# Optimization experiments

Hardware: AMD Instinct MI355X
Metric: run time of the kernel (lower is better)

The kernel has to match this reference:

```python
import jax, jax.numpy as jnp
import numpy as np

T, B, I, H = 512, 128, 256, 256
P = 0.25          # fixed dropout rate (float branch of p_logit)
EPS = 1e-07
TEMP = 0.1


def _concrete_mask(u, p):
    # (1 - sigmoid((log(p+eps)-log(1-p+eps)+log(u+eps)-log(1-u+eps))/t)) / (1-p)
    logit_p = jnp.log(p + EPS) - jnp.log(1.0 - p + EPS)
    logit_u = jnp.log(u + EPS) - jnp.log(1.0 - u + EPS)
    return (1.0 - jax.nn.sigmoid((logit_p + logit_u) / TEMP)) / (1.0 - p)


def setup_inputs() -> dict:
    key = jax.random.key(0)
    ks = jax.random.split(key, 7)
    k_scale = 1.0 / np.sqrt(H)  # matches uniform(-k, k) scale in init_weights
    inp = {
        "input": jax.random.normal(ks[0], (T, B, I), dtype=jnp.float32),
        "ux": jax.random.uniform(ks[1], (4, B, I), dtype=jnp.float32),
        "uh": jax.random.uniform(ks[2], (4, B, H), dtype=jnp.float32),
        "W": jax.random.normal(ks[3], (4, H, I), dtype=jnp.float32) * k_scale,
        "Wb": jax.random.normal(ks[4], (4, H), dtype=jnp.float32) * k_scale,
        "U": jax.random.normal(ks[5], (4, H, H), dtype=jnp.float32) * k_scale,
        "Ub": jax.random.normal(ks[6], (4, H), dtype=jnp.float32) * k_scale,
    }
    return inp


def reference(input, ux, uh, W, Wb, U, Ub):
    # Dropout masks (sampled once, shared across all timesteps), gate order i,f,o,g
    zx = _concrete_mask(ux, P)  # (4, B, I)
    zh = _concrete_mask(uh, P)  # (4, B, H)

    # Input-side gate pre-activations for ALL timesteps at once:
    # x_g[t] = (input[t] * zx[g]) @ W[g].T + Wb[g]  -> (T, B, 4, H)
    xm = input[:, None, :, :] * zx[None]                 # (T, 4, B, I)
    x_pre = jnp.einsum("tgbi,ghi->tbgh", xm, W) + Wb     # (T, B, 4, H)

    h0 = jnp.zeros((B, H), dtype=input.dtype)
    c0 = jnp.zeros((B, H), dtype=input.dtype)

    def step(carry, pre_t):
        h, c = carry
        hm = h[None] * zh                                 # (4, B, H)
        s = pre_t + jnp.einsum("gbh,gkh->bgk", hm, U) + Ub  # (B, 4, H)
        i = jax.nn.sigmoid(s[:, 0])
        f = jax.nn.sigmoid(s[:, 1])
        o = jax.nn.sigmoid(s[:, 2])
        g = jnp.tanh(s[:, 3])
        c = f * c + i * g
        h = o * jnp.tanh(c)
        return (h, c), h

    (h_t, c_t), hn = jax.lax.scan(step, (h0, c0), x_pre)
    return hn, h_t, c_t
```

## Files before the change

### kernel.cpp

```cpp
#include <hip/hip_runtime.h>
#include <hip/hip_bf16.h>

#define T_STEPS 512
#define B_SZ    128
#define I_SZ    256
#define H_SZ    256
#define NB      16
#define SCAN_BLOCKS (B_SZ / NB)
#define SCAN_THREADS 512

typedef __attribute__((ext_vector_type(8))) short short8;
typedef __attribute__((ext_vector_type(4))) float floatx4;
union I4S8 { uint4 u; short8 s; };

#define HM_G_STRIDE 8320
#define ST_OFF      33280
#define ST_ROW      268
#define ULDS_OFF    (ST_OFF + 64 * ST_ROW * 4)
#define ULDS_W      7168
#define SMEM_BYTES  (ULDS_OFF + 8 * ULDS_W)

static constexpr int SORD[8][8] = {
    {-1,-1,-1,-1,-1, 0, 2, 4},
    {-1,-1,-1,-1,-1, 1, 3, 5},
    {-1,-1,-1,-1,-1, 6, 8,10},
    {-1,-1,-1,-1,-1, 7, 9,11},
    {-1,-1,-1,-1,-1,12,14,16},
    {-1,-1,-1,-1,-1,13,15,17},
    {-1,-1,-1,-1,-1,19,21,23},
    {-1,-1,-1,-1,18,20,22,24},
};
static constexpr int SFRG[25] = {
     5,13, 6,14, 7,15,
    21,29,22,30,23,31,
    37,45,38,46,39,47,
    60,53,61,54,62,55,63
};

__device__ __forceinline__ float fast_sigmoid(float x) {
    return 1.f / (1.f + __expf(-x));
}
__device__ __forceinline__ float fast_tanh(float x) {
    float ax = fabsf(x);
    float e = __expf(-2.f * ax);
    float t = (1.f - e) / (1.f + e);
    return copysignf(t, x);
}
__device__ __forceinline__ ushort f2bf(float v) {
    __hip_bfloat16 hb = __float2bfloat16(v);
    return *(ushort*)&hb;
}
__device__ __forceinline__ float bf2f(ushort u) {
    unsigned int b = ((unsigned int)u) << 16;
    return __uint_as_float(b);
}
__device__ __forceinline__ float concrete_mask(float u) {
    const float EPS = 1e-7f;
    float logit_p = logf(0.25f + EPS) - logf(0.75f + EPS);
    float lu = logf(u + EPS) - logf(1.0f - u + EPS);
    float z = (logit_p + lu) * 10.0f;
    float sig = 1.0f / (1.0f + expf(-z));
    return (1.0f - sig) * (1.0f / 0.75f);
}

__device__ __forceinline__ void barrier_lds_only() {
    asm volatile("s_waitcnt lgkmcnt(0)" ::: "memory");
    __builtin_amdgcn_s_barrier();
    asm volatile("" ::: "memory");
}

__global__ void mask_kernel(const float* __restrict__ ux, const float* __restrict__ uh,
                            float* __restrict__ zx, __hip_bfloat16* __restrict__ zh) {
    int idx = blockIdx.x * blockDim.x + threadIdx.x;
    const int n = 4 * B_SZ * I_SZ;
    if (idx < n) zx[idx] = concrete_mask(ux[idx]);
    else         zh[idx - n] = __float2bfloat16(concrete_mask(uh[idx - n]));
}

__global__ void uswz_kernel(const float* __restrict__ M, __hip_bfloat16* __restrict__ M_sw) {
    int tId = blockIdx.x * 256 + threadIdx.x;
    int lane  = tId & 63;
    int kk    = (tId >> 6) & 7;
    int ktile = (tId >> 9) & 15;
    int g     = tId >> 13;
    int nCol  = ktile * 16 + (lane & 15);
    int h0    = kk * 32 + ((lane >> 4) & 3) * 8;
    const float* src = M + ((size_t)g * 256 + nCol) * 256 + h0;
    ushort o[8];
    #pragma unroll
    for (int j = 0; j < 8; ++j) o[j] = f2bf(src[j]);
    uint4 pk;
    pk.x = (uint)o[0] | ((uint)o[1] << 16);
    pk.y = (uint)o[2] | ((uint)o[3] << 16);
    pk.z = (uint)o[4] | ((uint)o[5] << 16);
    pk.w = (uint)o[6] | ((uint)o[7] << 16);
    ((uint4*)M_sw)[tId] = pk;
}

__global__ __launch_bounds__(512, 2) void xpre_mfma_kernel(
        const float* __restrict__ input, const float* __restrict__ zx,
        const __hip_bfloat16* __restrict__ W_sw,
        const float* __restrict__ Wb, const float* __restrict__ Ub,
        __hip_bfloat16* __restrict__ xpre) {
    const int tid   = threadIdx.x;
    const int w     = tid >> 6;
    const int lane  = tid & 63;
    const int g     = w >> 1;
    const int khalf = w & 1;
    const int row0  = blockIdx.x * 64;
    const int mrow  = lane & 15;
    const int kq    = lane >> 4;

    floatx4 acc[4][8];
    #pragma unroll
    for (int mt = 0; mt < 4; ++mt)
        #pragma unroll
        for (int nt = 0; nt < 8; ++nt)
            #pragma unroll
            for (int r = 0; r < 4; ++r) acc[mt][nt][r] = 0.f;

    const uint4* Wp = (const uint4*)W_sw + ((size_t)((g * 16 + khalf * 8) * 8)) * 64 + lane;

    for (int kc = 0; kc < 8; ++kc) {
        I4S8 af[4];
        const int i0 = kc * 32 + kq * 8;
        #pragma unroll
        for (int mt = 0; mt < 4; ++mt) {
            int row = row0 + mt * 16 + mrow;
            int b   = row & (B_SZ - 1);
            const float4* ip = (const float4*)(input + (size_t)row * I_SZ + i0);
            const float4* zp = (const float4*)(zx + ((size_t)g * B_SZ + b) * I_SZ + i0);
            float4 a0 = ip[0], a1 = ip[1];
            float4 z0 = zp[0], z1 = zp[1];
            uint4 pk;
            pk.x = (uint)f2bf(a0.x * z0.x) | ((uint)f2bf(a0.y * z0.y) << 16);
            pk.y = (uint)f2bf(a0.z * z0.z) | ((uint)f2bf(a0.w * z0.w) << 16);
            pk.z = (uint)f2bf(a1.x * z1.x) | ((uint)f2bf(a1.y * z1.y) << 16);
            pk.w = (uint)f2bf(a1.z * z1.z) | ((uint)f2bf(a1.w * z1.w) << 16);
            af[mt].u = pk;
        }
        #pragma unroll
        for (int nt = 0; nt < 8; ++nt) {
            I4S8 bb; bb.u = Wp[(nt * 8 + kc) * 64];
            #pragma unroll
            for (int mt = 0; mt < 4; ++mt)
                acc[mt][nt] = __builtin_amdgcn_mfma_f32_16x16x32_bf16(af[mt].s, bb.s, acc[mt][nt], 0, 0, 0);
        }
    }
    #pragma unroll
    for (int nt = 0; nt < 8; ++nt) {
        int col = khalf * 128 + nt * 16 + (lane & 15);
        float bias = Wb[g * H_SZ + col] + Ub[g * H_SZ + col];
        #pragma unroll
        for (int mt = 0; mt < 4; ++mt) {
            #pragma unroll
            for (int r = 0; r < 4; ++r) {
                int row = row0 + mt * 16 + (lane >> 4) * 4 + r;
                xpre[((size_t)row * 4 + g) * H_SZ + col] = __float2bfloat16(acc[mt][nt][r] + bias);
            }
        }
    }
}

__global__ __launch_bounds__(SCAN_THREADS, 2) void scan_mfma_kernel(
        const __hip_bfloat16* __restrict__ xpre,
        const __hip_bfloat16* __restrict__ zh,
        const __hip_bfloat16* __restrict__ U_sw,
        float* __restrict__ out) {
    extern __shared__ __align__(16) char smem[];
    const int tid  = threadIdx.x;
    const int b0   = blockIdx.x * NB;
    const int w     = tid >> 6;
    const int lane  = tid & 63;
    const int g_w   = w >> 1;
    const int khalf = w & 1;
    const int be      = tid >> 5;
    const int k8      = (tid & 31) * 8;
    const int kk_e    = k8 >> 5;
    const int lane_hm = (be & 15) | (((k8 >> 3) & 3) << 4);
    const int sw_e    = ((be >> 2) & 1) << 4;

    const uint4* Uw = (const uint4*)U_sw + ((size_t)((g_w * 16 + khalf * 8) * 8)) * 64 + lane;
    float* st = (float*)(smem + ST_OFF);

    uint4 ures[32];
    #pragma unroll
    for (int nt = 0; nt < 8; ++nt)
        #pragma unroll
        for (int kk = 0; kk < 4; ++kk)
            ures[nt * 4 + kk] = Uw[(nt * 8 + kk) * 64];
    #pragma unroll
    for (int f = 0; f < 7; ++f) {
        uint4 v = Uw[(f * 8 + 4) * 64];
        *(uint4*)(smem + ULDS_OFF + w * ULDS_W + f * 1024 + lane * 16) = v;
    }
    for (int i = tid; i < HM_G_STRIDE * 4 / 16; i += SCAN_THREADS)
        ((uint4*)smem)[i] = make_uint4(0u, 0u, 0u, 0u);

    uint4 zhreg[4];
    float c8[8], h8[8];
    #pragma unroll
    for (int g = 0; g < 4; ++g)
        zhreg[g] = *(const uint4*)(zh + ((size_t)g * B_SZ + (b0 + be)) * H_SZ + k8);
    #pragma unroll
    for (int j = 0; j < 8; ++j) c8[j] = 0.f;

    uint4 xpn[4];
    #pragma unroll
    for (int g = 0; g < 4; ++g)
        xpn[g] = *(const uint4*)(xpre + (((size_t)0 * B_SZ + (b0 + be)) * 4 + g) * H_SZ + k8);
    uint4 sbuf[4];
    #pragma unroll
    for (int q = 0; q < 4; ++q) sbuf[q] = Uw[SFRG[q] * 64];

    __syncthreads();

    for (int t = 0; t < T_STEPS; ++t) {
        I4S8 afr[8];
        #pragma unroll
        for (int kk = 0; kk < 8; ++kk)
            afr[kk].u = *(const uint4*)(smem + g_w * HM_G_STRIDE + kk * 1040 + lane * 16);

        #pragma unroll
        for (int p = 0; p < 4; ++p) {
            floatx4 acc[2];
            #pragma unroll
            for (int e = 0; e < 2; ++e)
                #pragma unroll
                for (int r = 0; r < 4; ++r) acc[e][r] = 0.f;

            uint4 lb[2];
            #pragma unroll
            for (int e = 0; e < 2; ++e) {
                const int nt = 2 * p + e;
                if (nt < 7)
                    lb[e] = *(const uint4*)(smem + ULDS_OFF + w * ULDS_W + nt * 1024 + lane * 16);
            }

            #pragma unroll
            for (int kk = 0; kk < 8; ++kk) {
                #pragma unroll
                for (int e = 0; e < 2; ++e) {
                    const int nt = 2 * p + e;
                    I4S8 bb;
                    if (kk < 4) {
                        bb.u = ures[nt * 4 + kk];
                    } else if (kk == 4 && nt < 7) {
                        bb.u = lb[e];
                    } else {
                        const int o = SORD[nt][kk];
                        bb.u = sbuf[o & 3];
                        if (o + 4 < 25) sbuf[o & 3] = Uw[SFRG[o + 4] * 64];
                    }
                    acc[e] = __builtin_amdgcn_mfma_f32_16x16x32_bf16(afr[kk].s, bb.s, acc[e], 0, 0, 0);
                }
            }
            #pragma unroll
            for (int e = 0; e < 2; ++e) {
                const int nt = 2 * p + e;
                int kcol  = khalf * 128 + nt * 16 + (lane & 15);
                int kswz  = kcol ^ (((lane >> 4) & 1) << 4);
                int brow4 = (lane >> 4) * 4;
                #pragma unroll
                for (int r = 0; r < 4; ++r)
                    st[((brow4 + r) * 4 + g_w) * ST_ROW + kswz] = acc[e][r];
            }
        }
        barrier_lds_only();

        float sg[4][8];
        #pragma unroll
        for (int g = 0; g < 4; ++g) {
            const float* strow = st + ((be * 4 + g) * ST_ROW + (k8 ^ sw_e));
            float4 lo = *(const float4*)(strow);
            float4 hi = *(const float4*)(strow + 4);
            sg[g][0] = lo.x; sg[g][1] = lo.y; sg[g][2] = lo.z; sg[g][3] = lo.w;
            sg[g][4] = hi.x; sg[g][5] = hi.y; sg[g][6] = hi.z; sg[g][7] = hi.w;
            const ushort* xs = (const ushort*)&xpn[g];
            #pragma unroll
            for (int j = 0; j < 8; ++j) sg[g][j] += bf2f(xs[j]);
        }
        {
            const int tn = (t + 1 < T_STEPS) ? t + 1 : t;
            #pragma unroll
            for (int g = 0; g < 4; ++g)
                xpn[g] = *(const uint4*)(xpre + (((size_t)tn * B_SZ + (b0 + be)) * 4 + g) * H_SZ + k8);
        }
        #pragma unroll
        for (int j = 0; j < 8; ++j) {
            float iv = fast_sigmoid(sg[0][j]);
            float fv = fast_sigmoid(sg[1][j]);
            float ov = fast_sigmoid(sg[2][j]);
            float gv = fast_tanh(sg[3][j]);
            float c  = fv * c8[j] + iv * gv;
            c8[j] = c;
            h8[j] = ov * fast_tanh(c);
        }
        {
            float* op = out + ((size_t)t * B_SZ + (b0 + be)) * H_SZ + k8;
            *(float4*)(op)     = make_float4(h8[0], h8[1], h8[2], h8[3]);
            *(float4*)(op + 4) = make_float4(h8[4], h8[5], h8[6], h8[7]);
        }
        #pragma unroll
        for (int g = 0; g < 4; ++g) {
            const ushort* zs = (const ushort*)&zhreg[g];
            uint4 pk;
            pk.x = (uint)f2bf(h8[0] * bf2f(zs[0])) | ((uint)f2bf(h8[1] * bf2f(zs[1])) << 16);
            pk.y = (uint)f2bf(h8[2] * bf2f(zs[2])) | ((uint)f2bf(h8[3] * bf2f(zs[3])) << 16);
            pk.z = (uint)f2bf(h8[4] * bf2f(zs[4])) | ((uint)f2bf(h8[5] * bf2f(zs[5])) << 16);
            pk.w = (uint)f2bf(h8[6] * bf2f(zs[6])) | ((uint)f2bf(h8[7] * bf2f(zs[7])) << 16);
            *(uint4*)(smem + g * HM_G_STRIDE + kk_e * 1040 + lane_hm * 16) = pk;
        }
        #pragma unroll
        for (int q = 0; q < 4; ++q) sbuf[q] = Uw[SFRG[q] * 64];

        if (t == T_STEPS - 1) {
            size_t tail = (size_t)T_STEPS * B_SZ * H_SZ;
            float* hp = out + tail + (size_t)(b0 + be) * H_SZ + k8;
            float* cp = hp + (size_t)B_SZ * H_SZ;
            *(float4*)(hp)     = make_float4(h8[0], h8[1], h8[2], h8[3]);
            *(float4*)(hp + 4) = make_float4(h8[4], h8[5], h8[6], h8[7]);
            *(float4*)(cp)     = make_float4(c8[0], c8[1], c8[2], c8[3]);
            *(float4*)(cp + 4) = make_float4(c8[4], c8[5], c8[6], c8[7]);
        }
        barrier_lds_only();
    }
}

extern "C" void kernel_launch(void* const* d_in, const int* in_sizes, int n_in,
                              void* d_out, int out_size, void* d_ws, size_t ws_size,
                              hipStream_t stream) {
    const float* input = (const float*)d_in[0];
    const float* ux    = (const float*)d_in[1];
    const float* uh    = (const float*)d_in[2];
    const float* W     = (const float*)d_in[3];
    const float* Wb    = (const float*)d_in[4];
    const float* U     = (const float*)d_in[5];
    const float* Ub    = (const float*)d_in[6];
    float* out = (float*)d_out;

    float* zx            = (float*)d_ws;
    __hip_bfloat16* zh   = (__hip_bfloat16*)(zx + 4 * B_SZ * I_SZ);
    __hip_bfloat16* U_sw = zh + 4 * B_SZ * H_SZ;
    __hip_bfloat16* W_sw = U_sw + 4 * H_SZ * H_SZ;
    __hip_bfloat16* xpre = W_sw + 4 * H_SZ * I_SZ;

    mask_kernel<<<dim3(1024), dim3(256), 0, stream>>>(ux, uh, zx, zh);
    uswz_kernel<<<dim3(128), dim3(256), 0, stream>>>(U, U_sw);
    uswz_kernel<<<dim3(128), dim3(256), 0, stream>>>(W, W_sw);

    xpre_mfma_kernel<<<dim3(1024), dim3(512), 0, stream>>>(input, zx, W_sw, Wb, Ub, xpre);

    scan_mfma_kernel<<<dim3(SCAN_BLOCKS), dim3(SCAN_THREADS), SMEM_BYTES, stream>>>(
        xpre, zh, U_sw, out);
}
```

Before: 4.608 ms.

## Prefetch x_pre via global_load_lds and shrink LDS-resident U fragments

Next-step x_pre gate values are now loaded asynchronously straight into a per-wave LDS buffer with global_load_lds, then read back from LDS after the barrier, instead of being held in registers. The LDS-cached U fragments per wave drop from 7 to 3, with more fragments streamed from global memory through a longer SORD/SFRG schedule. The custom LDS-only barriers are replaced by full __syncthreads, which also wait on the async global-to-LDS loads. The sbuf prefetch moves to the start of each step. Together these shift register and LDS pressure, at the cost of more global U traffic per step and heavier barriers.

Measured after the change: 4.758 ms. 1.03x slower.

```diff
diff --git a/kernel.cpp b/kernel.cpp
--- a/kernel.cpp
+++ b/kernel.cpp
@@ -17,24 +17,25 @@
 #define ST_OFF      33280
 #define ST_ROW      268
 #define ULDS_OFF    (ST_OFF + 64 * ST_ROW * 4)
-#define ULDS_W      7168
-#define SMEM_BYTES  (ULDS_OFF + 8 * ULDS_W)
+#define ULDS_W      3072
+#define XPBUF_OFF   (ULDS_OFF + 8 * ULDS_W)
+#define SMEM_BYTES  (XPBUF_OFF + 8 * 4096)
 
 static constexpr int SORD[8][8] = {
     {-1,-1,-1,-1,-1, 0, 2, 4},
     {-1,-1,-1,-1,-1, 1, 3, 5},
-    {-1,-1,-1,-1,-1, 6, 8,10},
     {-1,-1,-1,-1,-1, 7, 9,11},
-    {-1,-1,-1,-1,-1,12,14,16},
-    {-1,-1,-1,-1,-1,13,15,17},
-    {-1,-1,-1,-1,-1,19,21,23},
-    {-1,-1,-1,-1,18,20,22,24},
+    {-1,-1,-1,-1, 6, 8,10,12},
+    {-1,-1,-1,-1,13,15,17,19},
+    {-1,-1,-1,-1,14,16,18,20},
+    {-1,-1,-1,-1,21,23,25,27},
+    {-1,-1,-1,-1,22,24,26,28},
 };
-static constexpr int SFRG[25] = {
+static constexpr int SFRG[29] = {
      5,13, 6,14, 7,15,
-    21,29,22,30,23,31,
-    37,45,38,46,39,47,
-    60,53,61,54,62,55,63
+    28,21,29,22,30,23,31,
+    36,44,37,45,38,46,39,47,
+    52,60,53,61,54,62,55,63
 };
 
 __device__ __forceinline__ float fast_sigmoid(float x) {
@@ -61,12 +62,6 @@
     float z = (logit_p + lu) * 10.0f;
     float sig = 1.0f / (1.0f + expf(-z));
     return (1.0f - sig) * (1.0f / 0.75f);
-}
-
-__device__ __forceinline__ void barrier_lds_only() {
-    asm volatile("s_waitcnt lgkmcnt(0)" ::: "memory");
-    __builtin_amdgcn_s_barrier();
-    asm volatile("" ::: "memory");
 }
 
 __global__ void mask_kernel(const float* __restrict__ ux, const float* __restrict__ uh,
@@ -182,6 +177,7 @@
 
     const uint4* Uw = (const uint4*)U_sw + ((size_t)((g_w * 16 + khalf * 8) * 8)) * 64 + lane;
     float* st = (float*)(smem + ST_OFF);
+    char* xpw = smem + XPBUF_OFF + w * 4096;
 
     uint4 ures[32];
     #pragma unroll
@@ -190,7 +186,7 @@
         for (int kk = 0; kk < 4; ++kk)
             ures[nt * 4 + kk] = Uw[(nt * 8 + kk) * 64];
     #pragma unroll
-    for (int f = 0; f < 7; ++f) {
+    for (int f = 0; f < 3; ++f) {
         uint4 v = Uw[(f * 8 + 4) * 64];
         *(uint4*)(smem + ULDS_OFF + w * ULDS_W + f * 1024 + lane * 16) = v;
     }
@@ -205,13 +201,14 @@
     #pragma unroll
     for (int j = 0; j < 8; ++j) c8[j] = 0.f;
 
-    uint4 xpn[4];
-    #pragma unroll
-    for (int g = 0; g < 4; ++g)
-        xpn[g] = *(const uint4*)(xpre + (((size_t)0 * B_SZ + (b0 + be)) * 4 + g) * H_SZ + k8);
-    uint4 sbuf[4];
-    #pragma unroll
-    for (int q = 0; q < 4; ++q) sbuf[q] = Uw[SFRG[q] * 64];
+    #pragma unroll
+    for (int g = 0; g < 4; ++g) {
+        const void* src = (const void*)(xpre + (((size_t)0 * B_SZ + (b0 + be)) * 4 + g) * H_SZ + k8);
+        __builtin_amdgcn_global_load_lds(
+            (const __attribute__((address_space(1))) void*)src,
+            (__attribute__((address_space(3))) void*)(xpw + g * 1024),
+            16, 0, 0);
+    }
 
     __syncthreads();
 
@@ -220,6 +217,10 @@
         #pragma unroll
         for (int kk = 0; kk < 8; ++kk)
             afr[kk].u = *(const uint4*)(smem + g_w * HM_G_STRIDE + kk * 1040 + lane * 16);
+
+        uint4 sbuf[4];
+        #pragma unroll
+        for (int q = 0; q < 4; ++q) sbuf[q] = Uw[SFRG[q] * 64];
 
         #pragma unroll
         for (int p = 0; p < 4; ++p) {
@@ -233,7 +234,7 @@
             #pragma unroll
             for (int e = 0; e < 2; ++e) {
                 const int nt = 2 * p + e;
-                if (nt < 7)
+                if (nt < 3)
                     lb[e] = *(const uint4*)(smem + ULDS_OFF + w * ULDS_W + nt * 1024 + lane * 16);
             }
 
@@ -245,12 +246,12 @@
                     I4S8 bb;
                     if (kk < 4) {
                         bb.u = ures[nt * 4 + kk];
-                    } else if (kk == 4 && nt < 7) {
+                    } else if (kk == 4 && nt < 3) {
                         bb.u = lb[e];
                     } else {
                         const int o = SORD[nt][kk];
                         bb.u = sbuf[o & 3];
-                        if (o + 4 < 25) sbuf[o & 3] = Uw[SFRG[o + 4] * 64];
+                        if (o + 4 < 29) sbuf[o & 3] = Uw[SFRG[o + 4] * 64];
                     }
                     acc[e] = __builtin_amdgcn_mfma_f32_16x16x32_bf16(afr[kk].s, bb.s, acc[e], 0, 0, 0);
                 }
@@ -266,7 +267,12 @@
                     st[((brow4 + r) * 4 + g_w) * ST_ROW + kswz] = acc[e][r];
             }
         }
-        barrier_lds_only();
+        __syncthreads();
+
+        uint4 xpn[4];
+        #pragma unroll
+        for (int g = 0; g < 4; ++g)
+            xpn[g] = *(const uint4*)(xpw + g * 1024 + lane * 16);
 
         float sg[4][8];
         #pragma unroll
@@ -283,8 +289,13 @@
         {
             const int tn = (t + 1 < T_STEPS) ? t + 1 : t;
             #pragma unroll
-            for (int g = 0; g < 4; ++g)
-                xpn[g] = *(const uint4*)(xpre + (((size_t)tn * B_SZ + (b0 + be)) * 4 + g) * H_SZ + k8);
+            for (int g = 0; g < 4; ++g) {
+                const void* src = (const void*)(xpre + (((size_t)tn * B_SZ + (b0 + be)) * 4 + g) * H_SZ + k8);
+                __builtin_amdgcn_global_load_lds(
+                    (const __attribute__((address_space(1))) void*)src,
+                    (__attribute__((address_space(3))) void*)(xpw + g * 1024),
+                    16, 0, 0);
+            }
         }
         #pragma unroll
         for (int j = 0; j < 8; ++j) {
@@ -311,9 +322,6 @@
             pk.w = (uint)f2bf(h8[6] * bf2f(zs[6])) | ((uint)f2bf(h8[7] * bf2f(zs[7])) << 16);
             *(uint4*)(smem + g * HM_G_STRIDE + kk_e * 1040 + lane_hm * 16) = pk;
         }
-        #pragma unroll
-        for (int q = 0; q < 4; ++q) sbuf[q] = Uw[SFRG[q] * 64];
-
         if (t == T_STEPS - 1) {
             size_t tail = (size_t)T_STEPS * B_SZ * H_SZ;
             float* hp = out + tail + (size_t)(b0 + be) * H_SZ + k8;
@@ -323,7 +331,7 @@
             *(float4*)(cp)     = make_float4(c8[0], c8[1], c8[2], c8[3]);
             *(float4*)(cp + 4) = make_float4(c8[4], c8[5], c8[6], c8[7]);
         }
-        barrier_lds_only();
+        __syncthreads();
     }
 }
 
```
